# Performance work log

Measured on AMD Instinct MI355X. Metric: run time of the kernel, lower is better.

## Reference

```python
import jax, jax.numpy as jnp
import numpy as np

B, L, P, D, C, S = 32768, 256, 1024, 50, 3, 10  # batch, latent, n_protos, proto_size, classes, slots/class
EPS = 1e-5
IN_EPS = 1e-5  # torch InstanceNorm1d default eps


def _instance_norm(h):
    # torch InstanceNorm1d on (N, 50): unbatched (C, L) semantics -> normalize each row
    # over the feature axis with biased variance, no affine.
    m = jnp.mean(h, axis=-1, keepdims=True)
    v = jnp.mean((h - m) ** 2, axis=-1, keepdims=True)
    return (h - m) * jax.lax.rsqrt(v + IN_EPS)


def _project(z, W1, b1, W2, b2):
    # Linear(256->50) -> InstanceNorm1d -> ReLU -> Linear(50->50)
    h = z @ W1.T + b1
    h = jax.nn.relu(_instance_norm(h))
    return h @ W2.T + b2


def setup_inputs() -> dict:
    key = jax.random.key(0)
    ks = jax.random.split(key, 6)
    x = jax.random.normal(ks[0], (B, L), dtype=jnp.float32)
    prototypes = jax.random.normal(ks[1], (P, L), dtype=jnp.float32)
    # xavier_normal_(gain=1) on (C, P, S): std = sqrt(2 / (fan_in + fan_out)) = sqrt(2/(P+S))
    proto_presence = jax.random.normal(ks[2], (C, P, S), dtype=jnp.float32) * np.sqrt(2.0 / (P + S)).astype(np.float32)
    W1 = jax.random.normal(ks[3], (D, L), dtype=jnp.float32) * np.sqrt(1.0 / L).astype(np.float32)
    b1 = jnp.zeros((D,), jnp.float32)
    W2 = jax.random.normal(ks[4], (D, D), dtype=jnp.float32) * np.sqrt(1.0 / D).astype(np.float32)
    b2 = jnp.zeros((D,), jnp.float32)
    # class_identity_layer weight: Wc[c, i] = 1 if i // S == c else 0  -> (C, C*S)
    Wc = jnp.asarray((np.arange(C * S) // S == np.arange(C)[:, None]).astype(np.float32))
    return {"x": x, "gumbel_scalar": 0, "prototypes": prototypes,
            "proto_presence": proto_presence, "W1": W1, "b1": b1,
            "W2": W2, "b2": b2, "Wc": Wc}


def reference(x, gumbel_scalar, prototypes, proto_presence, W1, b1, W2, b2, Wc):
    # routing weights over prototypes (dim=1)
    if gumbel_scalar == 0:
        pp = jax.nn.softmax(proto_presence, axis=1)
    else:
        u = jax.random.uniform(jax.random.key(1), proto_presence.shape,
                               minval=1e-20, maxval=1.0, dtype=proto_presence.dtype)
        g = -jnp.log(-jnp.log(u))
        pp = jax.nn.softmax((proto_presence * gumbel_scalar + g) / 0.5, axis=1)

    xp = _project(x, W1, b1, W2, b2)            # [B, 50]
    lp = _project(prototypes, W1, b1, W2, b2)   # [P, 50] (batched per-prototype loop; row-wise InstanceNorm is identical)

    # L2 distance via ||a-b||^2 = ||a||^2 + ||b||^2 - 2 a.b (single GEMM instead of [B,50,P] broadcast)
    l2 = (jnp.sum(xp * xp, axis=-1)[:, None]
          + jnp.sum(lp * lp, axis=-1)[None, :]
          - 2.0 * (xp @ lp.T))                  # [B, P]
    l2 = jnp.maximum(l2, 0.0)  # clamp tiny negative fp residue; exact math is >= 0

    similarity = jnp.log((l2 + 1.0) / (l2 + EPS))          # [B, P]
    mixed = jnp.einsum('bp,cpn->bcn', similarity, pp)      # [B, C, S]
    out1 = mixed.reshape(x.shape[0], -1) @ Wc.T            # [B, C]
    out2 = jnp.concatenate([jnp.tanh(out1[:, :1]), jax.nn.relu(out1[:, 1:])], axis=1)
    return (out2, xp, similarity, pp)
```

## Files before the change

### kernel.cpp

```cpp
#include <hip/hip_runtime.h>
#include <cmath>

#define Bn 32768
#define Ln 256
#define Pn 1024
#define Dn 50
#define Cn 3
#define Sn 10

__global__ void pp_softmax_kernel(const float* __restrict__ pres, float* __restrict__ pp) {
    int c = blockIdx.x / Sn;
    int n = blockIdx.x % Sn;
    int lane = threadIdx.x;
    const float* src = pres + (size_t)c * Pn * Sn + n;
    float* dst = pp + (size_t)c * Pn * Sn + n;
    float v[16];
    float mx = -1e30f;
#pragma unroll
    for (int i = 0; i < 16; ++i) { v[i] = src[(size_t)(lane + i * 64) * Sn]; mx = fmaxf(mx, v[i]); }
#pragma unroll
    for (int m = 1; m < 64; m <<= 1) mx = fmaxf(mx, __shfl_xor(mx, m, 64));
    float sum = 0.f;
#pragma unroll
    for (int i = 0; i < 16; ++i) { v[i] = __expf(v[i] - mx); sum += v[i]; }
#pragma unroll
    for (int m = 1; m < 64; m <<= 1) sum += __shfl_xor(sum, m, 64);
    float inv = 1.0f / sum;
#pragma unroll
    for (int i = 0; i < 16; ++i) dst[(size_t)(lane + i * 64) * Sn] = v[i] * inv;
}

__global__ void pp_rowsum_kernel(const float* __restrict__ pp, float* __restrict__ pps) {
    int idx = blockIdx.x * blockDim.x + threadIdx.x;
    if (idx < Cn * Pn) {
        float s = 0.f;
#pragma unroll
        for (int n = 0; n < Sn; ++n) s += pp[(size_t)idx * Sn + n];
        pps[idx] = s;
    }
}

__global__ __launch_bounds__(256) void project_kernel(
    const float* __restrict__ zin,
    const float* __restrict__ W1, const float* __restrict__ b1,
    const float* __restrict__ W2, const float* __restrict__ b2,
    float* __restrict__ outp, float* __restrict__ outn, int rowsPerWave)
{
    __shared__ float w1s[Dn][Ln + 1];
    __shared__ float w2s[Dn][Dn + 1];
    __shared__ float zs[4][4][Ln];
    __shared__ float rs[4][4][Dn + 2];

    int t = threadIdx.x;
    for (int idx = t; idx < Dn * Ln; idx += 256) w1s[idx >> 8][idx & (Ln - 1)] = W1[idx];
    for (int idx = t; idx < Dn * Dn; idx += 256) w2s[idx / Dn][idx % Dn] = W2[idx];
    int wave = t >> 6, lane = t & 63;
    int jj = lane < Dn ? lane : 0;
    bool act = lane < Dn;
    float rb1 = b1[jj], rb2 = b2[jj];
    __syncthreads();

    int rowBase = (blockIdx.x * 4 + wave) * rowsPerWave;
    for (int rr = 0; rr < rowsPerWave; rr += 4) {
        int row0 = rowBase + rr;
#pragma unroll
        for (int r = 0; r < 4; ++r)
#pragma unroll
            for (int i = 0; i < 4; ++i)
                zs[wave][r][lane + i * 64] = zin[(size_t)(row0 + r) * Ln + lane + i * 64];
        __syncthreads();

        float h0 = rb1, h1 = rb1, h2 = rb1, h3 = rb1;
#pragma unroll 4
        for (int k = 0; k < Ln; ++k) {
            float w = w1s[jj][k];
            h0 += zs[wave][0][k] * w;
            h1 += zs[wave][1][k] * w;
            h2 += zs[wave][2][k] * w;
            h3 += zs[wave][3][k] * w;
        }
        float hh[4] = {h0, h1, h2, h3};
#pragma unroll
        for (int r = 0; r < 4; ++r) {
            float h = hh[r];
            float s = act ? h : 0.f;
#pragma unroll
            for (int m = 1; m < 64; m <<= 1) s += __shfl_xor(s, m, 64);
            float mean = s * (1.0f / Dn);
            float dv = act ? (h - mean) : 0.f;
            float s2 = dv * dv;
#pragma unroll
            for (int m = 1; m < 64; m <<= 1) s2 += __shfl_xor(s2, m, 64);
            float var = s2 * (1.0f / Dn);
            float rv = fmaxf((h - mean) * rsqrtf(var + 1e-5f), 0.f);
            if (act) rs[wave][r][lane] = rv;
        }
        __syncthreads();

        float o0 = rb2, o1 = rb2, o2 = rb2, o3 = rb2;
#pragma unroll 2
        for (int k = 0; k < Dn; ++k) {
            float w = w2s[jj][k];
            o0 += rs[wave][0][k] * w;
            o1 += rs[wave][1][k] * w;
            o2 += rs[wave][2][k] * w;
            o3 += rs[wave][3][k] * w;
        }
        float oo[4] = {o0, o1, o2, o3};
#pragma unroll
        for (int r = 0; r < 4; ++r) {
            float o = oo[r];
            if (act) outp[(size_t)(row0 + r) * Dn + lane] = o;
            float q = act ? o * o : 0.f;
#pragma unroll
            for (int m = 1; m < 64; m <<= 1) q += __shfl_xor(q, m, 64);
            if (lane == 0) outn[row0 + r] = q;
        }
        __syncthreads();
    }
}

__global__ __launch_bounds__(256) void sim_kernel(
    const float* __restrict__ xp, const float* __restrict__ xpn,
    const float* __restrict__ lp, const float* __restrict__ lpn,
    const float* __restrict__ ppsum,
    float* __restrict__ sim, float* __restrict__ out2)
{
    __shared__ float xs[64][53];
    __shared__ float ls[128][53];
    __shared__ float lns[128];
    __shared__ float pps[Cn * Pn];

    int t = threadIdx.x;
    int tx = t & 15, ty = t >> 4;
    int row0 = blockIdx.x * 64;

    for (int idx = t; idx < 64 * Dn; idx += 256) {
        int r = idx / Dn, c = idx - r * Dn;
        xs[r][c] = xp[(size_t)(row0 + r) * Dn + c];
    }
    for (int idx = t; idx < Cn * Pn; idx += 256) pps[idx] = ppsum[idx];

    float xn[4];
#pragma unroll
    for (int i = 0; i < 4; ++i) xn[i] = xpn[row0 + ty * 4 + i];

    float oacc[3][4] = {};

    for (int pt = 0; pt < Pn / 128; ++pt) {
        int p0 = pt * 128;
        __syncthreads();
        for (int idx = t; idx < 128 * Dn; idx += 256) {
            int r = idx / Dn, c = idx - r * Dn;
            ls[r][c] = lp[(size_t)(p0 + r) * Dn + c];
        }
        if (t < 128) lns[t] = lpn[p0 + t];
        __syncthreads();

        float acc[4][8];
#pragma unroll
        for (int i = 0; i < 4; ++i)
#pragma unroll
            for (int q = 0; q < 8; ++q) acc[i][q] = 0.f;

#pragma unroll 2
        for (int k = 0; k < Dn; ++k) {
            float xv[4], lv[8];
#pragma unroll
            for (int i = 0; i < 4; ++i) xv[i] = xs[ty * 4 + i][k];
#pragma unroll
            for (int g = 0; g < 2; ++g)
#pragma unroll
                for (int j = 0; j < 4; ++j) lv[g * 4 + j] = ls[g * 64 + tx * 4 + j][k];
#pragma unroll
            for (int i = 0; i < 4; ++i)
#pragma unroll
                for (int q = 0; q < 8; ++q) acc[i][q] += xv[i] * lv[q];
        }

#pragma unroll
        for (int i = 0; i < 4; ++i) {
            int row = row0 + ty * 4 + i;
#pragma unroll
            for (int g = 0; g < 2; ++g) {
                float4 sv;
#pragma unroll
                for (int j = 0; j < 4; ++j) {
                    int pl = g * 64 + tx * 4 + j;
                    float l2 = xn[i] + lns[pl] - 2.f * acc[i][g * 4 + j];
                    l2 = fmaxf(l2, 0.f);
                    float sval = __logf(__fdividef(l2 + 1.f, l2 + 1e-5f));
                    (&sv.x)[j] = sval;
                    const float* ppc = &pps[p0 + pl];
                    oacc[0][i] += sval * ppc[0];
                    oacc[1][i] += sval * ppc[Pn];
                    oacc[2][i] += sval * ppc[2 * Pn];
                }
                *reinterpret_cast<float4*>(sim + (size_t)row * Pn + p0 + g * 64 + tx * 4) = sv;
            }
        }
    }

#pragma unroll
    for (int c = 0; c < 3; ++c)
#pragma unroll
        for (int i = 0; i < 4; ++i) {
            float v = oacc[c][i];
            v += __shfl_xor(v, 1, 64);
            v += __shfl_xor(v, 2, 64);
            v += __shfl_xor(v, 4, 64);
            v += __shfl_xor(v, 8, 64);
            if (tx == 0) {
                int row = row0 + ty * 4 + i;
                out2[(size_t)row * 3 + c] = (c == 0) ? tanhf(v) : fmaxf(v, 0.f);
            }
        }
}

extern "C" void kernel_launch(void* const* d_in, const int* in_sizes, int n_in,
                              void* d_out, int out_size, void* d_ws, size_t ws_size,
                              hipStream_t stream) {
    const float* x    = (const float*)d_in[0];
    const float* prot = (const float*)d_in[2];
    const float* pres = (const float*)d_in[3];
    const float* W1   = (const float*)d_in[4];
    const float* b1   = (const float*)d_in[5];
    const float* W2   = (const float*)d_in[6];
    const float* b2   = (const float*)d_in[7];

    float* out  = (float*)d_out;
    float* out2 = out;
    float* xp   = out + (size_t)Bn * Cn;
    float* sim  = xp + (size_t)Bn * Dn;
    float* pp   = sim + (size_t)Bn * Pn;

    float* ws    = (float*)d_ws;
    float* lpbuf = ws;
    float* lpn   = lpbuf + Pn * Dn;
    float* xpn   = lpn + Pn;
    float* pps   = xpn + Bn;

    hipLaunchKernelGGL(pp_softmax_kernel, dim3(Cn * Sn), dim3(64), 0, stream, pres, pp);
    hipLaunchKernelGGL(pp_rowsum_kernel, dim3((Cn * Pn + 255) / 256), dim3(256), 0, stream, pp, pps);
    hipLaunchKernelGGL(project_kernel, dim3(Bn / 32), dim3(256), 0, stream,
                       x, W1, b1, W2, b2, xp, xpn, 8);
    hipLaunchKernelGGL(project_kernel, dim3(Pn / 32), dim3(256), 0, stream,
                       prot, W1, b1, W2, b2, lpbuf, lpn, 8);
    hipLaunchKernelGGL(sim_kernel, dim3(Bn / 64), dim3(256), 0, stream,
                       xp, xpn, lpbuf, lpn, pps, sim, out2);
}
```

Before: 346.3 us.

## Use bf16 MFMA for distance GEMM and retile projection as register-blocked GEMM

Projection kernel is rewritten as a 64-row tiled register-blocked GEMM with transposed weights in shared memory, and it also emits bf16 copies of projected vectors padded to 64. The similarity kernel now uses bf16 MFMA 16x16x32 for the dot products and splits prototypes across waves. The class outputs are accumulated with atomics and finished by a separate finalize kernel. This trades fp32 dot-product accuracy for matrix-core throughput and adds atomics, a memset and an extra launch. Similarity stores are now scalar and strided per lane rather than float4.

After: 325.2 us. 6.1% less time.

```diff
diff --git a/kernel.cpp b/kernel.cpp
--- a/kernel.cpp
+++ b/kernel.cpp
@@ -7,6 +7,15 @@
 #define Dn 50
 #define Cn 3
 #define Sn 10
+
+typedef short bf16x8 __attribute__((ext_vector_type(8)));
+typedef float f32x4 __attribute__((ext_vector_type(4)));
+
+__device__ inline unsigned short f2bf(float f) {
+    unsigned int u = __float_as_uint(f);
+    unsigned int r = (u + 0x7FFFu + ((u >> 16) & 1u)) >> 16;
+    return (unsigned short)r;
+}
 
 __global__ void pp_softmax_kernel(const float* __restrict__ pres, float* __restrict__ pp) {
     int c = blockIdx.x / Sn;
@@ -44,177 +53,212 @@
     const float* __restrict__ zin,
     const float* __restrict__ W1, const float* __restrict__ b1,
     const float* __restrict__ W2, const float* __restrict__ b2,
-    float* __restrict__ outp, float* __restrict__ outn, int rowsPerWave)
+    float* __restrict__ outp, float* __restrict__ outn,
+    unsigned short* __restrict__ outb)
 {
-    __shared__ float w1s[Dn][Ln + 1];
-    __shared__ float w2s[Dn][Dn + 1];
-    __shared__ float zs[4][4][Ln];
-    __shared__ float rs[4][4][Dn + 2];
-
-    int t = threadIdx.x;
-    for (int idx = t; idx < Dn * Ln; idx += 256) w1s[idx >> 8][idx & (Ln - 1)] = W1[idx];
-    for (int idx = t; idx < Dn * Dn; idx += 256) w2s[idx / Dn][idx % Dn] = W2[idx];
-    int wave = t >> 6, lane = t & 63;
-    int jj = lane < Dn ? lane : 0;
-    bool act = lane < Dn;
-    float rb1 = b1[jj], rb2 = b2[jj];
-    __syncthreads();
-
-    int rowBase = (blockIdx.x * 4 + wave) * rowsPerWave;
-    for (int rr = 0; rr < rowsPerWave; rr += 4) {
-        int row0 = rowBase + rr;
-#pragma unroll
-        for (int r = 0; r < 4; ++r)
-#pragma unroll
-            for (int i = 0; i < 4; ++i)
-                zs[wave][r][lane + i * 64] = zin[(size_t)(row0 + r) * Ln + lane + i * 64];
-        __syncthreads();
-
-        float h0 = rb1, h1 = rb1, h2 = rb1, h3 = rb1;
-#pragma unroll 4
-        for (int k = 0; k < Ln; ++k) {
-            float w = w1s[jj][k];
-            h0 += zs[wave][0][k] * w;
-            h1 += zs[wave][1][k] * w;
-            h2 += zs[wave][2][k] * w;
-            h3 += zs[wave][3][k] * w;
-        }
-        float hh[4] = {h0, h1, h2, h3};
-#pragma unroll
-        for (int r = 0; r < 4; ++r) {
-            float h = hh[r];
-            float s = act ? h : 0.f;
-#pragma unroll
-            for (int m = 1; m < 64; m <<= 1) s += __shfl_xor(s, m, 64);
-            float mean = s * (1.0f / Dn);
-            float dv = act ? (h - mean) : 0.f;
-            float s2 = dv * dv;
-#pragma unroll
-            for (int m = 1; m < 64; m <<= 1) s2 += __shfl_xor(s2, m, 64);
-            float var = s2 * (1.0f / Dn);
-            float rv = fmaxf((h - mean) * rsqrtf(var + 1e-5f), 0.f);
-            if (act) rs[wave][r][lane] = rv;
-        }
-        __syncthreads();
-
-        float o0 = rb2, o1 = rb2, o2 = rb2, o3 = rb2;
-#pragma unroll 2
-        for (int k = 0; k < Dn; ++k) {
-            float w = w2s[jj][k];
-            o0 += rs[wave][0][k] * w;
-            o1 += rs[wave][1][k] * w;
-            o2 += rs[wave][2][k] * w;
-            o3 += rs[wave][3][k] * w;
-        }
-        float oo[4] = {o0, o1, o2, o3};
-#pragma unroll
-        for (int r = 0; r < 4; ++r) {
-            float o = oo[r];
-            if (act) outp[(size_t)(row0 + r) * Dn + lane] = o;
-            float q = act ? o * o : 0.f;
-#pragma unroll
-            for (int m = 1; m < 64; m <<= 1) q += __shfl_xor(q, m, 64);
-            if (lane == 0) outn[row0 + r] = q;
-        }
-        __syncthreads();
-    }
-}
-
-__global__ __launch_bounds__(256) void sim_kernel(
-    const float* __restrict__ xp, const float* __restrict__ xpn,
-    const float* __restrict__ lp, const float* __restrict__ lpn,
-    const float* __restrict__ ppsum,
-    float* __restrict__ sim, float* __restrict__ out2)
-{
-    __shared__ float xs[64][53];
-    __shared__ float ls[128][53];
-    __shared__ float lns[128];
-    __shared__ float pps[Cn * Pn];
+    __shared__ float xs[64][68];
+    __shared__ float w1t[64][68];
+    __shared__ float w2t[52][68];
 
     int t = threadIdx.x;
     int tx = t & 15, ty = t >> 4;
     int row0 = blockIdx.x * 64;
 
-    for (int idx = t; idx < 64 * Dn; idx += 256) {
-        int r = idx / Dn, c = idx - r * Dn;
-        xs[r][c] = xp[(size_t)(row0 + r) * Dn + c];
-    }
-    for (int idx = t; idx < Cn * Pn; idx += 256) pps[idx] = ppsum[idx];
-
-    float xn[4];
-#pragma unroll
-    for (int i = 0; i < 4; ++i) xn[i] = xpn[row0 + ty * 4 + i];
-
-    float oacc[3][4] = {};
-
-    for (int pt = 0; pt < Pn / 128; ++pt) {
-        int p0 = pt * 128;
+    for (int idx = t; idx < 52 * 64; idx += 256) {
+        int j = idx & 63, k = idx >> 6;
+        w2t[k][j] = (j < Dn && k < Dn) ? W2[j * Dn + k] : 0.f;
+    }
+
+    float acc[4][4] = {};
+    for (int kc = 0; kc < Ln; kc += 64) {
         __syncthreads();
-        for (int idx = t; idx < 128 * Dn; idx += 256) {
-            int r = idx / Dn, c = idx - r * Dn;
-            ls[r][c] = lp[(size_t)(p0 + r) * Dn + c];
-        }
-        if (t < 128) lns[t] = lpn[p0 + t];
+        for (int idx = t; idx < 64 * 64; idx += 256) {
+            int kk = idx & 63, r = idx >> 6;
+            xs[r][kk] = zin[(size_t)(row0 + r) * Ln + kc + kk];
+        }
+        for (int idx = t; idx < 64 * 64; idx += 256) {
+            int j = idx & 63, kk = idx >> 6;
+            w1t[kk][j] = (j < Dn) ? W1[j * Ln + kc + kk] : 0.f;
+        }
         __syncthreads();
-
-        float acc[4][8];
+#pragma unroll 4
+        for (int k4 = 0; k4 < 16; ++k4) {
+            float4 xv[4], wv[4];
+#pragma unroll
+            for (int i = 0; i < 4; ++i) xv[i] = *(const float4*)&xs[ty * 4 + i][k4 * 4];
+#pragma unroll
+            for (int kk = 0; kk < 4; ++kk) wv[kk] = *(const float4*)&w1t[k4 * 4 + kk][tx * 4];
+#pragma unroll
+            for (int i = 0; i < 4; ++i)
+#pragma unroll
+                for (int kk = 0; kk < 4; ++kk)
+#pragma unroll
+                    for (int j = 0; j < 4; ++j)
+                        acc[i][j] += (&xv[i].x)[kk] * (&wv[kk].x)[j];
+        }
+    }
+
+    float rb1[4], rb2[4];
+    bool valid[4];
+#pragma unroll
+    for (int j = 0; j < 4; ++j) {
+        int c = tx * 4 + j;
+        valid[j] = c < Dn;
+        rb1[j] = valid[j] ? b1[c] : 0.f;
+        rb2[j] = valid[j] ? b2[c] : 0.f;
+    }
+
+    __syncthreads();
+
+#pragma unroll
+    for (int i = 0; i < 4; ++i) {
+        float h[4];
+        float s = 0.f;
+#pragma unroll
+        for (int j = 0; j < 4; ++j) { h[j] = acc[i][j] + rb1[j]; s += h[j]; }
+#pragma unroll
+        for (int m = 1; m < 16; m <<= 1) s += __shfl_xor(s, m, 64);
+        float mean = s * (1.0f / Dn);
+        float s2 = 0.f;
+#pragma unroll
+        for (int j = 0; j < 4; ++j) { float dv = valid[j] ? (h[j] - mean) : 0.f; s2 += dv * dv; }
+#pragma unroll
+        for (int m = 1; m < 16; m <<= 1) s2 += __shfl_xor(s2, m, 64);
+        float rstd = rsqrtf(s2 * (1.0f / Dn) + 1e-5f);
+        float4 rv;
+#pragma unroll
+        for (int j = 0; j < 4; ++j)
+            (&rv.x)[j] = valid[j] ? fmaxf((h[j] - mean) * rstd, 0.f) : 0.f;
+        *(float4*)&xs[ty * 4 + i][tx * 4] = rv;
+    }
+    __syncthreads();
+
+    float acc2[4][4] = {};
+#pragma unroll 4
+    for (int k4 = 0; k4 < 13; ++k4) {
+        float4 xv[4], wv[4];
+#pragma unroll
+        for (int i = 0; i < 4; ++i) xv[i] = *(const float4*)&xs[ty * 4 + i][k4 * 4];
+#pragma unroll
+        for (int kk = 0; kk < 4; ++kk) wv[kk] = *(const float4*)&w2t[k4 * 4 + kk][tx * 4];
 #pragma unroll
         for (int i = 0; i < 4; ++i)
 #pragma unroll
-            for (int q = 0; q < 8; ++q) acc[i][q] = 0.f;
-
-#pragma unroll 2
-        for (int k = 0; k < Dn; ++k) {
-            float xv[4], lv[8];
-#pragma unroll
-            for (int i = 0; i < 4; ++i) xv[i] = xs[ty * 4 + i][k];
-#pragma unroll
-            for (int g = 0; g < 2; ++g)
-#pragma unroll
-                for (int j = 0; j < 4; ++j) lv[g * 4 + j] = ls[g * 64 + tx * 4 + j][k];
-#pragma unroll
-            for (int i = 0; i < 4; ++i)
-#pragma unroll
-                for (int q = 0; q < 8; ++q) acc[i][q] += xv[i] * lv[q];
-        }
-
-#pragma unroll
-        for (int i = 0; i < 4; ++i) {
-            int row = row0 + ty * 4 + i;
-#pragma unroll
-            for (int g = 0; g < 2; ++g) {
-                float4 sv;
-#pragma unroll
-                for (int j = 0; j < 4; ++j) {
-                    int pl = g * 64 + tx * 4 + j;
-                    float l2 = xn[i] + lns[pl] - 2.f * acc[i][g * 4 + j];
+            for (int kk = 0; kk < 4; ++kk)
+#pragma unroll
+                for (int j = 0; j < 4; ++j)
+                    acc2[i][j] += (&xv[i].x)[kk] * (&wv[kk].x)[j];
+    }
+
+#pragma unroll
+    for (int i = 0; i < 4; ++i) {
+        int row = row0 + ty * 4 + i;
+        float o[4];
+        float q = 0.f;
+#pragma unroll
+        for (int j = 0; j < 4; ++j) {
+            o[j] = acc2[i][j] + rb2[j];
+            if (valid[j]) q += o[j] * o[j];
+            if (valid[j]) outp[(size_t)row * Dn + tx * 4 + j] = o[j];
+        }
+        ushort4 ob;
+        ob.x = valid[0] ? f2bf(o[0]) : 0;
+        ob.y = valid[1] ? f2bf(o[1]) : 0;
+        ob.z = valid[2] ? f2bf(o[2]) : 0;
+        ob.w = valid[3] ? f2bf(o[3]) : 0;
+        *(ushort4*)&outb[(size_t)row * 64 + tx * 4] = ob;
+#pragma unroll
+        for (int m = 1; m < 16; m <<= 1) q += __shfl_xor(q, m, 64);
+        if (tx == 0) outn[row] = q;
+    }
+}
+
+__global__ __launch_bounds__(256) void sim_mfma_kernel(
+    const unsigned short* __restrict__ xpb, const unsigned short* __restrict__ lpb,
+    const float* __restrict__ xpn, const float* __restrict__ lpn,
+    const float* __restrict__ pps,
+    float* __restrict__ sim, float* __restrict__ out1)
+{
+    int t = threadIdx.x;
+    int w = t >> 6, l = t & 63;
+    int lr = l & 15, lg = l >> 4;
+    int row0 = blockIdx.x * 64;
+
+    bf16x8 af[4][2];
+#pragma unroll
+    for (int m = 0; m < 4; ++m)
+#pragma unroll
+        for (int ks = 0; ks < 2; ++ks)
+            af[m][ks] = *(const bf16x8*)&xpb[(size_t)(row0 + m * 16 + lr) * 64 + ks * 32 + lg * 8];
+
+    float xnr[4][4];
+#pragma unroll
+    for (int m = 0; m < 4; ++m)
+#pragma unroll
+        for (int i = 0; i < 4; ++i)
+            xnr[m][i] = xpn[row0 + m * 16 + lg * 4 + i];
+
+    float oacc[4][4][3] = {};
+
+    for (int pt = 0; pt < 4; ++pt) {
+#pragma unroll
+        for (int n = 0; n < 4; ++n) {
+            int pc = w * 256 + pt * 64 + n * 16;
+            bf16x8 bfr[2];
+#pragma unroll
+            for (int ks = 0; ks < 2; ++ks)
+                bfr[ks] = *(const bf16x8*)&lpb[(size_t)(pc + lr) * 64 + ks * 32 + lg * 8];
+            f32x4 acc[4];
+#pragma unroll
+            for (int m = 0; m < 4; ++m) { f32x4 z = {0.f, 0.f, 0.f, 0.f}; acc[m] = z; }
+#pragma unroll
+            for (int ks = 0; ks < 2; ++ks)
+#pragma unroll
+                for (int m = 0; m < 4; ++m)
+                    acc[m] = __builtin_amdgcn_mfma_f32_16x16x32_bf16(af[m][ks], bfr[ks], acc[m], 0, 0, 0);
+
+            float ln = lpn[pc + lr];
+            float pr0 = pps[pc + lr];
+            float pr1 = pps[Pn + pc + lr];
+            float pr2 = pps[2 * Pn + pc + lr];
+#pragma unroll
+            for (int m = 0; m < 4; ++m)
+#pragma unroll
+                for (int i = 0; i < 4; ++i) {
+                    float l2 = xnr[m][i] + ln - 2.f * acc[m][i];
                     l2 = fmaxf(l2, 0.f);
-                    float sval = __logf(__fdividef(l2 + 1.f, l2 + 1e-5f));
-                    (&sv.x)[j] = sval;
-                    const float* ppc = &pps[p0 + pl];
-                    oacc[0][i] += sval * ppc[0];
-                    oacc[1][i] += sval * ppc[Pn];
-                    oacc[2][i] += sval * ppc[2 * Pn];
+                    float s = __logf(__fdividef(l2 + 1.f, l2 + 1e-5f));
+                    sim[(size_t)(row0 + m * 16 + lg * 4 + i) * Pn + pc + lr] = s;
+                    oacc[m][i][0] += s * pr0;
+                    oacc[m][i][1] += s * pr1;
+                    oacc[m][i][2] += s * pr2;
                 }
-                *reinterpret_cast<float4*>(sim + (size_t)row * Pn + p0 + g * 64 + tx * 4) = sv;
+        }
+    }
+
+#pragma unroll
+    for (int m = 0; m < 4; ++m)
+#pragma unroll
+        for (int i = 0; i < 4; ++i)
+#pragma unroll
+            for (int c = 0; c < 3; ++c) {
+                float v = oacc[m][i][c];
+                v += __shfl_xor(v, 1, 64);
+                v += __shfl_xor(v, 2, 64);
+                v += __shfl_xor(v, 4, 64);
+                v += __shfl_xor(v, 8, 64);
+                if (lr == 0)
+                    atomicAdd(&out1[(size_t)(row0 + m * 16 + lg * 4 + i) * Cn + c], v);
             }
-        }
-    }
-
-#pragma unroll
-    for (int c = 0; c < 3; ++c)
-#pragma unroll
-        for (int i = 0; i < 4; ++i) {
-            float v = oacc[c][i];
-            v += __shfl_xor(v, 1, 64);
-            v += __shfl_xor(v, 2, 64);
-            v += __shfl_xor(v, 4, 64);
-            v += __shfl_xor(v, 8, 64);
-            if (tx == 0) {
-                int row = row0 + ty * 4 + i;
-                out2[(size_t)row * 3 + c] = (c == 0) ? tanhf(v) : fmaxf(v, 0.f);
-            }
-        }
+}
+
+__global__ void finalize_kernel(const float* __restrict__ o1, float* __restrict__ out2) {
+    int i = blockIdx.x * 256 + threadIdx.x;
+    if (i < Bn * Cn) {
+        float v = o1[i];
+        int c = i - (i / Cn) * Cn;
+        out2[i] = (c == 0) ? tanhf(v) : fmaxf(v, 0.f);
+    }
 }
 
 extern "C" void kernel_launch(void* const* d_in, const int* in_sizes, int n_in,
@@ -234,18 +278,24 @@
     float* sim  = xp + (size_t)Bn * Dn;
     float* pp   = sim + (size_t)Bn * Pn;
 
-    float* ws    = (float*)d_ws;
-    float* lpbuf = ws;
-    float* lpn   = lpbuf + Pn * Dn;
-    float* xpn   = lpn + Pn;
-    float* pps   = xpn + Bn;
-
+    float* ws     = (float*)d_ws;
+    float* out1ws = ws;
+    float* xpn    = out1ws + (size_t)Bn * Cn;
+    float* lpn    = xpn + Bn;
+    float* pps    = lpn + Pn;
+    float* lpf    = pps + Cn * Pn;
+    unsigned short* xpb = (unsigned short*)(lpf + Pn * Dn);
+    unsigned short* lpb = xpb + (size_t)Bn * 64;
+
+    hipMemsetAsync(out1ws, 0, (size_t)Bn * Cn * sizeof(float), stream);
     hipLaunchKernelGGL(pp_softmax_kernel, dim3(Cn * Sn), dim3(64), 0, stream, pres, pp);
     hipLaunchKernelGGL(pp_rowsum_kernel, dim3((Cn * Pn + 255) / 256), dim3(256), 0, stream, pp, pps);
-    hipLaunchKernelGGL(project_kernel, dim3(Bn / 32), dim3(256), 0, stream,
-                       x, W1, b1, W2, b2, xp, xpn, 8);
-    hipLaunchKernelGGL(project_kernel, dim3(Pn / 32), dim3(256), 0, stream,
-                       prot, W1, b1, W2, b2, lpbuf, lpn, 8);
-    hipLaunchKernelGGL(sim_kernel, dim3(Bn / 64), dim3(256), 0, stream,
-                       xp, xpn, lpbuf, lpn, pps, sim, out2);
-}
+    hipLaunchKernelGGL(project_kernel, dim3(Bn / 64), dim3(256), 0, stream,
+                       x, W1, b1, W2, b2, xp, xpn, xpb);
+    hipLaunchKernelGGL(project_kernel, dim3(Pn / 64), dim3(256), 0, stream,
+                       prot, W1, b1, W2, b2, lpf, lpn, lpb);
+    hipLaunchKernelGGL(sim_mfma_kernel, dim3(Bn / 64), dim3(256), 0, stream,
+                       xpb, lpb, xpn, lpn, pps, sim, out1ws);
+    hipLaunchKernelGGL(finalize_kernel, dim3((Bn * Cn + 255) / 256), dim3(256), 0, stream,
+                       out1ws, out2);
+}
```
